# Optimization experiments

Hardware: AMD Instinct MI355X
Metric: run time of the kernel (lower is better)

The kernel has to match this reference:

```python
import jax, jax.numpy as jnp
import numpy as np

NUM_HEADS = 12
SS_ATTN_ITER = 1
EPS = 1e-12  # F.normalize default eps


def _l2norm(x):
    n = jnp.linalg.norm(x, axis=-1, keepdims=True)
    return x / jnp.maximum(n, EPS)


def setup_inputs() -> dict:
    key = jax.random.key(0)
    k1, k2, k3, k4 = jax.random.split(key, 4)
    N, B, C = 1569, 8, 768
    x = jax.random.normal(k1, (N, B, C), dtype=jnp.float32)
    Wqkv = jax.random.normal(k2, (3 * C, C), dtype=jnp.float32) * 0.02
    Wproj = jax.random.normal(k3, (C, C), dtype=jnp.float32) * 0.02
    bproj = jax.random.normal(k4, (C,), dtype=jnp.float32) * 0.02
    return {"x": x, "Wqkv": Wqkv, "Wproj": Wproj, "bproj": bproj}


def _forward(x, Wqkv, Wproj, bproj):
    # x: [N, B, C] -> [B, N, C] (module does x.transpose(0, 1))
    xb = jnp.swapaxes(x, 0, 1)
    B, N, C = xb.shape
    H = NUM_HEADS
    hd = C // H
    scale = hd ** (-0.5)

    # qkv projection (no bias), split into per-head q, k, v: [B, H, N, hd]
    qkv = (xb @ Wqkv.T).reshape(B, N, 3, H, hd)
    qkv = jnp.transpose(qkv, (2, 0, 3, 1, 4))
    q, k, v = qkv[0], qkv[1], qkv[2]

    # ---- original attention branch ----
    attn_ori = jax.nn.softmax(jnp.einsum('bhnd,bhmd->bhnm', q, k) * scale, axis=-1)
    x_ori = jnp.einsum('bhnm,bhmd->bhnd', attn_ori, v)
    x_ori = jnp.transpose(x_ori, (0, 2, 1, 3)).reshape(B, N, C)
    x_ori = x_ori @ Wproj.T + bproj

    # ---- self-self attention branches ----
    # inv_temp = mean over tokens of ||x||_2, per batch: [B, 1, 1, 1]
    pre_norm = jnp.mean(jnp.linalg.norm(xb, axis=-1), axis=-1)
    inv_temp = pre_norm[:, None, None, None] * scale

    def branch(xs):
        for _ in range(SS_ATTN_ITER):
            xs = _l2norm(xs)
            a = jax.nn.softmax(jnp.einsum('bhnd,bhmd->bhnm', xs, xs) * inv_temp, axis=-1)
            xs = jnp.einsum('bhnm,bhmd->bhnd', a, xs)
        xs = _l2norm(xs)
        a = jax.nn.softmax(jnp.einsum('bhnd,bhmd->bhnm', xs, xs) * inv_temp, axis=-1)
        return jnp.einsum('bhnm,bhmd->bhnd', a, v)

    xs = (branch(v) + branch(k) + branch(q)) / 3.0
    x_out = jnp.transpose(xs, (0, 2, 1, 3)).reshape(B, N, C)
    x_out = x_out @ Wproj.T + bproj

    # return in original [N, B, C] layout
    return jnp.swapaxes(x_out, 0, 1), jnp.swapaxes(x_ori, 0, 1)


def reference(x, Wqkv, Wproj, bproj):
    return _forward(x, Wqkv, Wproj, bproj)
```

## Files before the change

kernel.cpp:

```cpp
#include <hip/hip_runtime.h>
#include <stdint.h>

#define NTOK 1569
#define BB 8
#define CC 768
#define HH 12
#define HD 64
#define NBH (BB*HH)
#define NROW (NTOK*BB)
#define NCHUNK 25
#define NVEC (NBH*NTOK)
#define LASTV 33

typedef unsigned short ushort_t;
static const size_t SZ = (size_t)NROW * CC;

using f32x4 = __attribute__((ext_vector_type(4))) float;
using i32x4 = __attribute__((ext_vector_type(4))) int;
using i32x2 = __attribute__((ext_vector_type(2))) int;
using hfrag = __attribute__((ext_vector_type(8))) _Float16;

__device__ __forceinline__ float exp2_fast(float x){
  float r;
  asm("v_exp_f32 %0, %1" : "=v"(r) : "v"(x));
  return r;
}

__global__ __launch_bounds__(256) void prenorm_kernel(const float* __restrict__ x,
                                                      float* __restrict__ pre)
{
  const int b = blockIdx.y;
  const int wave = threadIdx.x >> 6, lane = threadIdx.x & 63;
  const int g = blockIdx.x * 4 + wave;
  float local = 0.f;
  for (int n = g; n < NTOK; n += 200){
    const float* xp = x + ((size_t)n * BB + b) * CC + lane * 4;
    float ss = 0.f;
    #pragma unroll
    for (int e = 0; e < 3; e++){
      f32x4 vv = *(const f32x4*)(xp + 256*e);
      ss += vv[0]*vv[0] + vv[1]*vv[1] + vv[2]*vv[2] + vv[3]*vv[3];
    }
    #pragma unroll
    for (int off = 1; off < 64; off <<= 1) ss += __shfl_xor(ss, off);
    local += sqrtf(ss);
  }
  if (lane == 0) atomicAdd(&pre[b], local);
}

__global__ __launch_bounds__(256) void cvt_f16(const float* __restrict__ in,
                                               ushort_t* __restrict__ out,
                                               int n8, float scl)
{
  const int i = blockIdx.x * 256 + threadIdx.x;
  if (i >= n8) return;
  const float* p = in + (size_t)i * 8;
  f32x4 a = *(const f32x4*)p, b = *(const f32x4*)(p + 4);
  union { _Float16 h[8]; i32x4 v; } u;
  #pragma unroll
  for (int e = 0; e < 4; e++){
    u.h[e]   = (_Float16)(a[e] * scl);
    u.h[4+e] = (_Float16)(b[e] * scl);
  }
  *(i32x4*)(out + (size_t)i * 8) = u.v;
}

__global__ __launch_bounds__(256) void gemm768(
    const ushort_t* __restrict__ A, const ushort_t* __restrict__ Bm,
    ushort_t* __restrict__ q, ushort_t* __restrict__ k, ushort_t* __restrict__ v,
    float* __restrict__ outp, const float* __restrict__ bias, int mode)
{
  __shared__ __align__(16) ushort_t As[8192];
  __shared__ __align__(16) ushort_t Bs[8192];

  const int jtN = gridDim.y;
  const int lin = blockIdx.y * 99 + blockIdx.x;
  const int T  = 99 * jtN;
  const int qq = T >> 3, rr = T & 7;
  const int c  = lin & 7, ii = lin >> 3;
  const int start = c*qq + (c < rr ? c : rr);
  const int idx = start + ii;
  const int mt = idx / jtN, jt = idx - mt*jtN;

  const int tid = threadIdx.x;
  const int w = tid >> 6, lane = tid & 63;
  const int l16 = lane & 15, lq = lane >> 4;

  const int srow = tid & 127, shalf = tid >> 7;
  int ga = mt*128 + srow; if (ga > NROW-1) ga = NROW-1;
  const ushort_t* ap = A  + (size_t)ga * CC + shalf*32;
  const ushort_t* bp = Bm + (size_t)(jt*128 + srow) * CC + shalf*32;
  const int rb = srow >> 4, r16 = srow & 15;

  const int wr = (w >> 1) * 4, wc = (w & 1) * 4;

  f32x4 acc[4][4] = {};
  for (int kt = 0; kt < 12; kt++){
    #pragma unroll
    for (int i = 0; i < 4; i++){
      const int kq = shalf*4 + i;
      *(i32x4*)&As[((rb*8 + kq)*16 + r16)*8] = *(const i32x4*)(ap + kt*64 + i*8);
      *(i32x4*)&Bs[((rb*8 + kq)*16 + r16)*8] = *(const i32x4*)(bp + kt*64 + i*8);
    }
    __syncthreads();
    #pragma unroll
    for (int ks = 0; ks < 2; ks++){
      hfrag af[4], bf[4];
      #pragma unroll
      for (int rt = 0; rt < 4; rt++)
        af[rt] = *(const hfrag*)&As[(((wr+rt)*8 + ks*4 + lq)*16 + l16)*8];
      #pragma unroll
      for (int ct = 0; ct < 4; ct++)
        bf[ct] = *(const hfrag*)&Bs[(((wc+ct)*8 + ks*4 + lq)*16 + l16)*8];
      #pragma unroll
      for (int rt = 0; rt < 4; rt++)
        #pragma unroll
        for (int ct = 0; ct < 4; ct++)
          acc[rt][ct] = __builtin_amdgcn_mfma_f32_16x16x32_f16(af[rt], bf[ct], acc[rt][ct], 0, 0, 0);
    }
    __syncthreads();
  }

  const int mbase = mt*128 + (w >> 1)*64;
  const int jbase = jt*128 + (w & 1)*64;
  #pragma unroll
  for (int ct = 0; ct < 4; ct++){
    const int j = jbase + ct*16 + l16;
    if (mode == 0){
      const int s = j / 768, jj = j - s*768;
      const int h = jj >> 6, d = jj & 63;
      ushort_t* op = (s == 0) ? q : (s == 1) ? k : v;
      #pragma unroll
      for (int rt = 0; rt < 4; rt++)
        #pragma unroll
        for (int r = 0; r < 4; r++){
          const int m = mbase + rt*16 + lq*4 + r;
          if (m < NROW){
            const int n = m >> 3, b = m & 7;
            union { _Float16 h16; ushort_t u; } cv;
            cv.h16 = (_Float16)acc[rt][ct][r];
            op[((size_t)(b*HH + h) * NTOK + n) * HD + d] = cv.u;
          }
        }
    } else {
      const float bv = bias[j];
      #pragma unroll
      for (int rt = 0; rt < 4; rt++)
        #pragma unroll
        for (int r = 0; r < 4; r++){
          const int m = mbase + rt*16 + lq*4 + r;
          if (m < NROW) outp[(size_t)m * CC + j] = acc[rt][ct][r] + bv;
        }
    }
  }
}

__global__ __launch_bounds__(256) void l2norm_kernel(const ushort_t* __restrict__ in,
                                                     ushort_t* __restrict__ out,
                                                     int mode)
{
  const int vec = blockIdx.x * 8 + (threadIdx.x >> 5);
  const int lane = threadIdx.x & 31;
  if (vec >= NVEC) return;
  size_t iaddr;
  if (mode == 0){
    iaddr = (size_t)vec * HD + lane*2;
  } else {
    const int b = vec / (HH*NTOK);
    const int rem = vec - b*(HH*NTOK);
    const int h = rem / NTOK, n = rem - h*NTOK;
    iaddr = (size_t)(n*BB + b) * CC + h*HD + lane*2;
  }
  union { ushort_t u[2]; uint32_t pk; _Float16 h[2]; } uv;
  uv.pk = *(const uint32_t*)(in + iaddr);
  const float a = (float)uv.h[0], c = (float)uv.h[1];
  float ss = a*a + c*c;
  #pragma unroll
  for (int off = 1; off < 32; off <<= 1) ss += __shfl_xor(ss, off);
  const float inv = 1.0f / fmaxf(sqrtf(ss), 1e-12f);
  union { _Float16 h[2]; uint32_t pk; } ov;
  ov.h[0] = (_Float16)(a * inv);
  ov.h[1] = (_Float16)(c * inv);
  *(uint32_t*)(out + (size_t)vec * HD + lane*2) = ov.pk;
}

__global__ __launch_bounds__(256) void attn_mfma(
    const ushort_t* __restrict__ X, const ushort_t* __restrict__ Y,
    const ushort_t* __restrict__ Z, void* __restrict__ outp,
    const float* __restrict__ pre, float tf, int mode, int accum)
{
  __shared__ __align__(16) ushort_t Ks[2][64*64];
  __shared__ __align__(16) ushort_t Vt[2][64*64];
  __shared__ __align__(16) ushort_t Pt[128*64];

  const int lin  = blockIdx.y * 13 + blockIdx.x;
  const int nl   = (lin & 7) * 156 + (lin >> 3);
  const int bh   = nl / 13;
  const int qblk = nl - bh * 13;

  const int b = bh / HH, h = bh - (bh / HH) * HH;
  const float temp = (pre ? pre[b] * tf : tf) * 1.4426950408889634f;
  const size_t base = (size_t)bh * NTOK * HD;
  const int row0 = qblk * 128;
  const int tid = threadIdx.x;
  const int w = tid >> 6, lane = tid & 63;
  const int l16 = lane & 15, lq = lane >> 4;
  const int xk = (l16 & 7) << 4;

  hfrag qf[2][2];
  #pragma unroll
  for (int qt = 0; qt < 2; qt++){
    int r = row0 + w*32 + qt*16 + l16; if (r > NTOK-1) r = NTOK-1;
    const ushort_t* qp = X + base + (size_t)r*HD + lq*8;
    qf[qt][0] = *(const hfrag*)qp;
    qf[qt][1] = *(const hfrag*)(qp + 32);
  }

  hfrag ones;
  #pragma unroll
  for (int e = 0; e < 8; e++) ones[e] = (_Float16)1.0f;

  const int skey = tid & 63, sseg = tid >> 6;
  const int kx = (skey & 7) << 4;
  const int vd2 = (tid & 31) * 2;
  const int vko = (tid >> 5) * 8;

  i32x4 kr0, kr1;
  uint32_t L[8];

  auto LOADR = [&](int ch){
    int kg = ch*64 + skey; if (kg > NTOK-1) kg = NTOK-1;
    const ushort_t* kp = Y + base + (size_t)kg*HD + sseg*16;
    kr0 = *(const i32x4*)kp;
    kr1 = *(const i32x4*)(kp + 8);
    #pragma unroll
    for (int j = 0; j < 8; j++){
      int vg = ch*64 + vko + j; if (vg > NTOK-1) vg = NTOK-1;
      L[j] = *(const uint32_t*)(Z + base + (size_t)vg*HD + vd2);
    }
  };
  auto STORER = [&](int bf){
    char* kbp = (char*)Ks[bf] + skey*128;
    *(i32x4*)(kbp + ((sseg*32     ) ^ kx)) = kr0;
    *(i32x4*)(kbp + ((sseg*32 + 16) ^ kx)) = kr1;
    i32x4 vlo, vhi;
    #pragma unroll
    for (int cc = 0; cc < 4; cc++){
      const uint32_t Aw = L[2*cc], Bw = L[2*cc+1];
      vlo[cc] = (int)((Aw & 0xffffu) | (Bw << 16));
      vhi[cc] = (int)((Aw >> 16) | (Bw & 0xffff0000u));
    }
    char* vbp = (char*)Vt[bf];
    *(i32x4*)(vbp + vd2*128     + ((vko*2) ^ ((vd2 & 7) << 4)))     = vlo;
    *(i32x4*)(vbp + (vd2+1)*128 + ((vko*2) ^ (((vd2+1) & 7) << 4))) = vhi;
  };

  f32x4 acc[2][4] = {};
  f32x4 acc1[2] = {};

  LOADR(0);
  STORER(0);
  __syncthreads();

  for (int ch = 0; ch < NCHUNK; ch++){
    const int cur = ch & 1;
    const char* Kc = (const char*)Ks[cur];
    const char* Vc = (const char*)Vt[cur];
    if (ch + 1 < NCHUNK) LOADR(ch + 1);

    const bool lastch = (ch == NCHUNK-1);
    #pragma unroll
    for (int kt4 = 0; kt4 < 4; kt4++){
      f32x4 s0 = {}, s1 = {};
      #pragma unroll
      for (int ks = 0; ks < 2; ks++){
        hfrag kf = *(const hfrag*)(Kc + (kt4*16 + l16)*128
                                   + ((ks*64 + lq*16) ^ xk));
        s0 = __builtin_amdgcn_mfma_f32_16x16x32_f16(kf, qf[0][ks], s0, 0, 0, 0);
        s1 = __builtin_amdgcn_mfma_f32_16x16x32_f16(kf, qf[1][ks], s1, 0, 0, 0);
      }
      const int kb = kt4*16 + lq*4;
      #pragma unroll
      for (int qt = 0; qt < 2; qt++){
        const f32x4 sv = qt ? s1 : s0;
        float p0 = exp2_fast(sv[0] * temp);
        float p1 = exp2_fast(sv[1] * temp);
        float p2 = exp2_fast(sv[2] * temp);
        float p3 = exp2_fast(sv[3] * temp);
        if (lastch){
          if (kb + 0 >= LASTV) p0 = 0.f;
          if (kb + 1 >= LASTV) p1 = 0.f;
          if (kb + 2 >= LASTV) p2 = 0.f;
          if (kb + 3 >= LASTV) p3 = 0.f;
        }
        union { _Float16 hh[4]; i32x2 v2; } pw;
        pw.hh[0] = (_Float16)p0; pw.hh[1] = (_Float16)p1;
        pw.hh[2] = (_Float16)p2; pw.hh[3] = (_Float16)p3;
        *(i32x2*)((char*)Pt + (w*32 + qt*16 + l16)*128
                  + ((kt4*32 + lq*8) ^ xk)) = pw.v2;
      }
    }

    #pragma unroll
    for (int ks = 0; ks < 2; ks++){
      const int cb = (ks*64 + lq*16) ^ xk;
      hfrag pa0 = *(const hfrag*)((const char*)Pt + (w*32 +      l16)*128 + cb);
      hfrag pa1 = *(const hfrag*)((const char*)Pt + (w*32 + 16 + l16)*128 + cb);
      #pragma unroll
      for (int dt4 = 0; dt4 < 4; dt4++){
        hfrag vf = *(const hfrag*)(Vc + (dt4*16 + l16)*128 + cb);
        acc[0][dt4] = __builtin_amdgcn_mfma_f32_16x16x32_f16(pa0, vf, acc[0][dt4], 0, 0, 0);
        acc[1][dt4] = __builtin_amdgcn_mfma_f32_16x16x32_f16(pa1, vf, acc[1][dt4], 0, 0, 0);
      }
      acc1[0] = __builtin_amdgcn_mfma_f32_16x16x32_f16(pa0, ones, acc1[0], 0, 0, 0);
      acc1[1] = __builtin_amdgcn_mfma_f32_16x16x32_f16(pa1, ones, acc1[1], 0, 0, 0);
    }

    if (ch + 1 < NCHUNK){
      STORER(cur ^ 1);
      __syncthreads();
    }
  }

  #pragma unroll
  for (int qt = 0; qt < 2; qt++)
    #pragma unroll
    for (int r = 0; r < 4; r++){
      const int n = row0 + w*32 + qt*16 + lq*4 + r;
      if (n < NTOK){
        const float inv = 1.0f / acc1[qt][r];
        const size_t rbase = (size_t)(n*BB + b) * CC + h*HD;
        if (mode == 0){
          ushort_t* yo = (ushort_t*)outp;
          #pragma unroll
          for (int dt4 = 0; dt4 < 4; dt4++){
            union { _Float16 h16; ushort_t u; } cv;
            cv.h16 = (_Float16)(acc[qt][dt4][r] * inv);
            yo[rbase + dt4*16 + l16] = cv.u;
          }
        } else {
          float* ao = (float*)outp;
          #pragma unroll
          for (int dt4 = 0; dt4 < 4; dt4++){
            float o = acc[qt][dt4][r] * inv;
            if (accum) o += ao[rbase + dt4*16 + l16];
            ao[rbase + dt4*16 + l16] = o;
          }
        }
      }
    }
}

extern "C" void kernel_launch(void* const* d_in, const int* in_sizes, int n_in,
                              void* d_out, int out_size, void* d_ws, size_t ws_size,
                              hipStream_t stream)
{
  (void)in_sizes; (void)n_in; (void)out_size; (void)ws_size;

  const float* x     = (const float*)d_in[0];
  const float* wqkv  = (const float*)d_in[1];
  const float* wproj = (const float*)d_in[2];
  const float* bias  = (const float*)d_in[3];
  float* out = (float*)d_out;

  ushort_t* x16  = (ushort_t*)d_ws;
  ushort_t* wq16 = x16 + SZ;
  ushort_t* wp16 = wq16 + (size_t)2304*768;
  ushort_t* qb   = wp16 + (size_t)768*768;
  ushort_t* kb   = qb + SZ;
  ushort_t* vb   = kb + SZ;
  ushort_t* xh   = vb + SZ;
  ushort_t* y16  = xh + SZ;
  float*    acc  = (float*)(y16 + SZ);
  float*    pre  = acc + SZ;

  hipMemsetAsync(pre, 0, BB * sizeof(float), stream);

  cvt_f16<<<(int)(SZ/8 + 255)/256, 256, 0, stream>>>(x, x16, (int)(SZ/8), 1.0f);
  cvt_f16<<<(2304*768/8 + 255)/256, 256, 0, stream>>>(wqkv, wq16, 2304*768/8, 1.0f);
  cvt_f16<<<(768*768/8 + 255)/256, 256, 0, stream>>>(wproj, wp16, 768*768/8, 1.0f);
  prenorm_kernel<<<dim3(50, 8), 256, 0, stream>>>(x, pre);

  gemm768<<<dim3(99, 18), 256, 0, stream>>>(x16, wq16, qb, kb, vb, nullptr, nullptr, 0);

  const float SCALE = 0.125f;
  const float FACT  = SCALE / (float)NTOK;
  const dim3 AG(13, 96);

  attn_mfma<<<AG, 256, 0, stream>>>(qb, kb, vb, y16, nullptr, SCALE, 0, 0);
  gemm768<<<dim3(99, 6), 256, 0, stream>>>(y16, wp16, nullptr, nullptr, nullptr,
      out + (size_t)NTOK * BB * CC, bias, 1);

  const ushort_t* srcs[3] = { qb, kb, vb };
  for (int sI = 0; sI < 3; sI++){
    l2norm_kernel<<<NVEC/8, 256, 0, stream>>>(srcs[sI], xh, 0);
    attn_mfma<<<AG, 256, 0, stream>>>(xh, xh, xh, y16, pre, FACT, 0, 0);
    l2norm_kernel<<<NVEC/8, 256, 0, stream>>>(y16, xh, 1);
    attn_mfma<<<AG, 256, 0, stream>>>(xh, xh, vb, acc, pre, FACT, 1, sI == 0 ? 0 : 1);
  }

  cvt_f16<<<(int)(SZ/8 + 255)/256, 256, 0, stream>>>(acc, y16, (int)(SZ/8), 1.0f/3.0f);
  gemm768<<<dim3(99, 6), 256, 0, stream>>>(y16, wp16, nullptr, nullptr, nullptr,
      out, bias, 1);
}
```

Before: 1.157 ms.

## Use direct global-to-LDS loads with XOR swizzle in GEMM; fuse final average into attention

Result: faster. 1.089 ms (-5.9%).

```diff
diff --git a/kernel.cpp b/kernel.cpp
--- a/kernel.cpp
+++ b/kernel.cpp
@@ -86,21 +86,34 @@
   const int w = tid >> 6, lane = tid & 63;
   const int l16 = lane & 15, lq = lane >> 4;
 
-  const int srow = tid & 127, shalf = tid >> 7;
-  int ga = mt*128 + srow; if (ga > NROW-1) ga = NROW-1;
-  const ushort_t* ap = A  + (size_t)ga * CC + shalf*32;
-  const ushort_t* bp = Bm + (size_t)(jt*128 + srow) * CC + shalf*32;
-  const int rb = srow >> 4, r16 = srow & 15;
+  const int rquad = lane >> 3;
+  const int kqs   = (lane & 7) ^ rquad;
+  const ushort_t* apb[4];
+  const ushort_t* bpb[4];
+  #pragma unroll
+  for (int i = 0; i < 4; i++){
+    int ar = mt*128 + i*32 + w*8 + rquad; if (ar > NROW-1) ar = NROW-1;
+    apb[i] = A + (size_t)ar*CC + kqs*8;
+    const int br = jt*128 + i*32 + w*8 + rquad;
+    bpb[i] = Bm + (size_t)br*CC + kqs*8;
+  }
 
   const int wr = (w >> 1) * 4, wc = (w & 1) * 4;
+  const int rx = l16 & 7;
 
   f32x4 acc[4][4] = {};
   for (int kt = 0; kt < 12; kt++){
     #pragma unroll
     for (int i = 0; i < 4; i++){
-      const int kq = shalf*4 + i;
-      *(i32x4*)&As[((rb*8 + kq)*16 + r16)*8] = *(const i32x4*)(ap + kt*64 + i*8);
-      *(i32x4*)&Bs[((rb*8 + kq)*16 + r16)*8] = *(const i32x4*)(bp + kt*64 + i*8);
+      __builtin_amdgcn_global_load_lds(
+          (const __attribute__((address_space(1))) void*)apb[i],
+          (__attribute__((address_space(3))) void*)&As[(i*256 + w*64)*8],
+          16, 0, 0);
+      __builtin_amdgcn_global_load_lds(
+          (const __attribute__((address_space(1))) void*)bpb[i],
+          (__attribute__((address_space(3))) void*)&Bs[(i*256 + w*64)*8],
+          16, 0, 0);
+      apb[i] += 64; bpb[i] += 64;
     }
     __syncthreads();
     #pragma unroll
@@ -108,10 +121,12 @@
       hfrag af[4], bf[4];
       #pragma unroll
       for (int rt = 0; rt < 4; rt++)
-        af[rt] = *(const hfrag*)&As[(((wr+rt)*8 + ks*4 + lq)*16 + l16)*8];
+        af[rt] = *(const hfrag*)((const char*)As
+                   + ((wr+rt)*16 + l16)*128 + ((((ks*4+lq) ^ rx)) << 4));
       #pragma unroll
       for (int ct = 0; ct < 4; ct++)
-        bf[ct] = *(const hfrag*)&Bs[(((wc+ct)*8 + ks*4 + lq)*16 + l16)*8];
+        bf[ct] = *(const hfrag*)((const char*)Bs
+                   + ((wc+ct)*16 + l16)*128 + ((((ks*4+lq) ^ rx)) << 4));
       #pragma unroll
       for (int rt = 0; rt < 4; rt++)
         #pragma unroll
@@ -187,6 +202,7 @@
 __global__ __launch_bounds__(256) void attn_mfma(
     const ushort_t* __restrict__ X, const ushort_t* __restrict__ Y,
     const ushort_t* __restrict__ Z, void* __restrict__ outp,
+    const float* __restrict__ accin,
     const float* __restrict__ pre, float tf, int mode, int accum)
 {
   __shared__ __align__(16) ushort_t Ks[2][64*64];
@@ -338,13 +354,23 @@
             cv.h16 = (_Float16)(acc[qt][dt4][r] * inv);
             yo[rbase + dt4*16 + l16] = cv.u;
           }
-        } else {
+        } else if (mode == 1){
           float* ao = (float*)outp;
           #pragma unroll
           for (int dt4 = 0; dt4 < 4; dt4++){
             float o = acc[qt][dt4][r] * inv;
             if (accum) o += ao[rbase + dt4*16 + l16];
             ao[rbase + dt4*16 + l16] = o;
+          }
+        } else {
+          ushort_t* yo = (ushort_t*)outp;
+          #pragma unroll
+          for (int dt4 = 0; dt4 < 4; dt4++){
+            const float o = (accin[rbase + dt4*16 + l16]
+                             + acc[qt][dt4][r] * inv) * (1.0f/3.0f);
+            union { _Float16 h16; ushort_t u; } cv;
+            cv.h16 = (_Float16)o;
+            yo[rbase + dt4*16 + l16] = cv.u;
           }
         }
       }
@@ -387,19 +413,21 @@
   const float FACT  = SCALE / (float)NTOK;
   const dim3 AG(13, 96);
 
-  attn_mfma<<<AG, 256, 0, stream>>>(qb, kb, vb, y16, nullptr, SCALE, 0, 0);
+  attn_mfma<<<AG, 256, 0, stream>>>(qb, kb, vb, y16, nullptr, nullptr, SCALE, 0, 0);
   gemm768<<<dim3(99, 6), 256, 0, stream>>>(y16, wp16, nullptr, nullptr, nullptr,
       out + (size_t)NTOK * BB * CC, bias, 1);
 
   const ushort_t* srcs[3] = { qb, kb, vb };
   for (int sI = 0; sI < 3; sI++){
     l2norm_kernel<<<NVEC/8, 256, 0, stream>>>(srcs[sI], xh, 0);
-    attn_mfma<<<AG, 256, 0, stream>>>(xh, xh, xh, y16, pre, FACT, 0, 0);
+    attn_mfma<<<AG, 256, 0, stream>>>(xh, xh, xh, y16, nullptr, pre, FACT, 0, 0);
     l2norm_kernel<<<NVEC/8, 256, 0, stream>>>(y16, xh, 1);
-    attn_mfma<<<AG, 256, 0, stream>>>(xh, xh, vb, acc, pre, FACT, 1, sI == 0 ? 0 : 1);
-  }
-
-  cvt_f16<<<(int)(SZ/8 + 255)/256, 256, 0, stream>>>(acc, y16, (int)(SZ/8), 1.0f/3.0f);
+    if (sI < 2)
+      attn_mfma<<<AG, 256, 0, stream>>>(xh, xh, vb, acc, nullptr, pre, FACT, 1, sI == 0 ? 0 : 1);
+    else
+      attn_mfma<<<AG, 256, 0, stream>>>(xh, xh, vb, y16, acc, pre, FACT, 2, 1);
+  }
+
   gemm768<<<dim3(99, 6), 256, 0, stream>>>(y16, wp16, nullptr, nullptr, nullptr,
       out, bias, 1);
 }
```
